# Performance work log

Measured on AMD Instinct MI355X. Metric: run time of the kernel, lower is better.

Reference implementation:

```python
import jax, jax.numpy as jnp
import numpy as np

N_EL = 19        # electrodes per graph (hardcoded in module)
N_EDGES = 342    # 19*18 directed edges per graph, no self-loops
N_GRAPHS = 1800
C_IN = 128
C_OUT = 128


def setup_inputs() -> dict:
    key = jax.random.key(0)
    k1, k2, k3 = jax.random.split(key, 3)
    N = N_GRAPHS * N_EL
    x = jax.random.normal(k1, (N, C_IN), dtype=jnp.float32)
    # block-structured edge_index: same 342-edge pattern in every 19-node graph
    src_b, dst_b = np.nonzero(~np.eye(N_EL, dtype=bool))  # all i != j pairs
    offs = (np.arange(N_GRAPHS) * N_EL)[:, None]
    src = (src_b[None, :] + offs).reshape(-1)
    dst = (dst_b[None, :] + offs).reshape(-1)
    edge_index = jnp.asarray(np.stack([src, dst]), dtype=jnp.int32)  # [2, E]
    # learnable params: edge_weights init 'ones'; GraphConv lin_rel (bias) + lin_root (no bias)
    edge_weights = jnp.ones((N_EDGES,), dtype=jnp.float32)
    W_rel = jax.random.normal(k2, (C_OUT, C_IN), dtype=jnp.float32) * 0.05
    b_rel = jnp.zeros((C_OUT,), dtype=jnp.float32)
    W_root = jax.random.normal(k3, (C_OUT, C_IN), dtype=jnp.float32) * 0.05
    return {"x": x, "edge_index": edge_index, "edge_weights": edge_weights,
            "W_rel": W_rel, "b_rel": b_rel, "W_root": W_root}


def reference(x, edge_index, edge_weights, W_rel, b_rel, W_root):
    # repeat per-graph edge weights across all graphs (torch .repeat == jnp.tile)
    E = edge_index.shape[1]
    rep = jnp.tile(edge_weights, E // edge_weights.shape[0])          # [E]
    src, dst = edge_index[0], edge_index[1]
    # GraphConv message passing: gather source features, scale, scatter-add to targets
    msg = x[src] * rep[:, None]                                       # [E, C_in]
    agg = jax.ops.segment_sum(msg, dst, num_segments=x.shape[0])      # [N, C_in]
    # out = lin_rel(agg) + lin_root(x)
    return agg @ W_rel.T + b_rel + x @ W_root.T
```

## Files before the change

### kernel.cpp

```cpp
#include <hip/hip_runtime.h>
#include <hip/hip_bf16.h>

#define GPB 4
#define ROWS 76
#define MP 80
#define LDK 264
#define EPG 342

typedef short short8 __attribute__((ext_vector_type(8)));
typedef float f32x4  __attribute__((ext_vector_type(4)));

__device__ __forceinline__ unsigned int f2bf(float f) {
    unsigned int u = __float_as_uint(f);
    return (u + 0x7fffu + ((u >> 16) & 1u)) >> 16;
}
__device__ __forceinline__ float bf2f(unsigned int h) {
    return __uint_as_float(h << 16);
}
__device__ __forceinline__ int pk2(float lo, float hi) {
    return (int)(f2bf(lo) | (f2bf(hi) << 16));
}

__global__ __launch_bounds__(256) void graphconv_mfma(
    const float* __restrict__ x,
    const int*   __restrict__ ei,
    const float* __restrict__ ew,
    const float* __restrict__ Wrel,
    const float* __restrict__ brel,
    const float* __restrict__ Wroot,
    float* __restrict__ out,
    int E_total)
{
    __shared__ __align__(16) unsigned short Amat[MP * LDK];
    __shared__ float adj[GPB][19][20];

    const int t    = threadIdx.x;
    const int lane = t & 63;
    const int wv   = t >> 6;
    const int g0   = blockIdx.x * GPB;

    const int lrow = lane & 15;
    const int kq   = (lane >> 4) * 8;
    const int colA = wv * 16 + lrow;
    const int colB = (wv + 4) * 16 + lrow;

    short8 bf[2][2][4];
    #pragma unroll
    for (int pass = 0; pass < 2; ++pass) {
        const float* W = pass ? Wroot : Wrel;
        #pragma unroll
        for (int ct = 0; ct < 2; ++ct) {
            const float* wr = W + (size_t)(ct ? colB : colA) * 128 + kq;
            #pragma unroll
            for (int ks = 0; ks < 4; ++ks) {
                const float4* p = (const float4*)(wr + ks * 32);
                float4 a = p[0], b = p[1];
                union { short8 s; int i[4]; } u;
                u.i[0] = pk2(a.x, a.y); u.i[1] = pk2(a.z, a.w);
                u.i[2] = pk2(b.x, b.y); u.i[3] = pk2(b.z, b.w);
                bf[pass][ct][ks] = u.s;
            }
        }
    }
    const float bias0 = brel[colA];
    const float bias1 = brel[colB];

    const float4* xg = (const float4*)(x + (size_t)g0 * 19 * 128);
    for (int idx = t; idx < ROWS * 32; idx += 256) {
        int row = idx >> 5, c4 = idx & 31;
        float4 v = xg[idx];
        int2 w; w.x = pk2(v.x, v.y); w.y = pk2(v.z, v.w);
        *(int2*)&Amat[row * LDK + 128 + c4 * 4] = w;
    }
    for (int i = t; i < GPB * 19 * 20; i += 256) ((float*)adj)[i] = 0.f;
    __syncthreads();

    for (int e = t; e < GPB * EPG; e += 256) {
        int g  = e / EPG;
        int te = e - g * EPG;
        int ge = g0 * EPG + e;
        int nb = (g0 + g) * 19;
        int sl = ei[ge] - nb;
        int dl = ei[E_total + ge] - nb;
        adj[g][dl][sl] = ew[te];
    }
    __syncthreads();

    for (int idx = t; idx < ROWS * 128; idx += 256) {
        int j = idx >> 7, c = idx & 127;
        int g = j / 19, jl = j - g * 19;
        int bg = g * 19;
        float s = 0.f;
        #pragma unroll
        for (int i = 0; i < 19; ++i)
            s += adj[g][jl][i] * bf2f(Amat[(bg + i) * LDK + 128 + c]);
        Amat[j * LDK + c] = (unsigned short)f2bf(s);
    }
    __syncthreads();

    float* ob = out + (size_t)blockIdx.x * ROWS * 128;
    #pragma unroll
    for (int rt = 0; rt < 5; ++rt) {
        f32x4 acc0 = {0.f, 0.f, 0.f, 0.f};
        f32x4 acc1 = {0.f, 0.f, 0.f, 0.f};
        const unsigned short* ar = Amat + (rt * 16 + lrow) * LDK + kq;
        #pragma unroll
        for (int ks = 0; ks < 8; ++ks) {
            short8 a = *(const short8*)(ar + ks * 32);
            int p = ks >> 2, k4 = ks & 3;
            acc0 = __builtin_amdgcn_mfma_f32_16x16x32_bf16(a, bf[p][0][k4], acc0, 0, 0, 0);
            acc1 = __builtin_amdgcn_mfma_f32_16x16x32_bf16(a, bf[p][1][k4], acc1, 0, 0, 0);
        }
        int rbase = rt * 16 + (lane >> 4) * 4;
        #pragma unroll
        for (int r = 0; r < 4; ++r) {
            int row = rbase + r;
            if (row < ROWS) {
                ob[row * 128 + colA] = acc0[r] + bias0;
                ob[row * 128 + colB] = acc1[r] + bias1;
            }
        }
    }
}

extern "C" void kernel_launch(void* const* d_in, const int* in_sizes, int n_in,
                              void* d_out, int out_size, void* d_ws, size_t ws_size,
                              hipStream_t stream) {
    const float* x     = (const float*)d_in[0];
    const int*   ei    = (const int*)d_in[1];
    const float* ew    = (const float*)d_in[2];
    const float* Wrel  = (const float*)d_in[3];
    const float* brel  = (const float*)d_in[4];
    const float* Wroot = (const float*)d_in[5];
    float* out = (float*)d_out;

    const int E_total  = in_sizes[1] / 2;
    const int n_graphs = E_total / EPG;
    const int n_blocks = n_graphs / GPB;

    graphconv_mfma<<<n_blocks, 256, 0, stream>>>(
        x, ei, ew, Wrel, brel, Wroot, out, E_total);
}
```

Before: 115.3 us.

## Halve graphs per block and vectorize neighbor aggregation over 8 channels

Result: faster. 106.8 us (-7.4%).

```diff
diff --git a/kernel.cpp b/kernel.cpp
--- a/kernel.cpp
+++ b/kernel.cpp
@@ -1,23 +1,20 @@
 #include <hip/hip_runtime.h>
 #include <hip/hip_bf16.h>
 
-#define GPB 4
-#define ROWS 76
-#define MP 80
+#define GPB 2
+#define ROWS 38
+#define MP 48
 #define LDK 264
 #define EPG 342
 
 typedef short short8 __attribute__((ext_vector_type(8)));
 typedef float f32x4  __attribute__((ext_vector_type(4)));
 
-__device__ __forceinline__ unsigned int f2bf(float f) {
+static __device__ __forceinline__ unsigned int f2bf(float f) {
     unsigned int u = __float_as_uint(f);
     return (u + 0x7fffu + ((u >> 16) & 1u)) >> 16;
 }
-__device__ __forceinline__ float bf2f(unsigned int h) {
-    return __uint_as_float(h << 16);
-}
-__device__ __forceinline__ int pk2(float lo, float hi) {
+static __device__ __forceinline__ int pk2(float lo, float hi) {
     return (int)(f2bf(lo) | (f2bf(hi) << 16));
 }
 
@@ -76,7 +73,7 @@
     __syncthreads();
 
     for (int e = t; e < GPB * EPG; e += 256) {
-        int g  = e / EPG;
+        int g  = (e >= EPG) ? 1 : 0;
         int te = e - g * EPG;
         int ge = g0 * EPG + e;
         int nb = (g0 + g) * 19;
@@ -86,21 +83,37 @@
     }
     __syncthreads();
 
-    for (int idx = t; idx < ROWS * 128; idx += 256) {
-        int j = idx >> 7, c = idx & 127;
-        int g = j / 19, jl = j - g * 19;
+    for (int idx = t; idx < ROWS * 16; idx += 256) {
+        int j = idx >> 4, c8 = idx & 15;
+        int g = (j >= 19) ? 1 : 0;
+        int jl = j - g * 19;
         int bg = g * 19;
-        float s = 0.f;
+        float acc[8];
         #pragma unroll
-        for (int i = 0; i < 19; ++i)
-            s += adj[g][jl][i] * bf2f(Amat[(bg + i) * LDK + 128 + c]);
-        Amat[j * LDK + c] = (unsigned short)f2bf(s);
+        for (int q = 0; q < 8; ++q) acc[q] = 0.f;
+        #pragma unroll 4
+        for (int i = 0; i < 19; ++i) {
+            float a = adj[g][jl][i];
+            int4 w = *(const int4*)&Amat[(bg + i) * LDK + 128 + c8 * 8];
+            acc[0] += a * __uint_as_float((unsigned)w.x << 16);
+            acc[1] += a * __uint_as_float((unsigned)w.x & 0xffff0000u);
+            acc[2] += a * __uint_as_float((unsigned)w.y << 16);
+            acc[3] += a * __uint_as_float((unsigned)w.y & 0xffff0000u);
+            acc[4] += a * __uint_as_float((unsigned)w.z << 16);
+            acc[5] += a * __uint_as_float((unsigned)w.z & 0xffff0000u);
+            acc[6] += a * __uint_as_float((unsigned)w.w << 16);
+            acc[7] += a * __uint_as_float((unsigned)w.w & 0xffff0000u);
+        }
+        int4 o;
+        o.x = pk2(acc[0], acc[1]); o.y = pk2(acc[2], acc[3]);
+        o.z = pk2(acc[4], acc[5]); o.w = pk2(acc[6], acc[7]);
+        *(int4*)&Amat[j * LDK + c8 * 8] = o;
     }
     __syncthreads();
 
     float* ob = out + (size_t)blockIdx.x * ROWS * 128;
     #pragma unroll
-    for (int rt = 0; rt < 5; ++rt) {
+    for (int rt = 0; rt < 3; ++rt) {
         f32x4 acc0 = {0.f, 0.f, 0.f, 0.f};
         f32x4 acc1 = {0.f, 0.f, 0.f, 0.f};
         const unsigned short* ar = Amat + (rt * 16 + lrow) * LDK + kq;
```

## Reorder GraphConv as A·(X·Wrel) and precompute bf16 weights in a separate kernel

Applied to the files above, without the earlier changes.

Result: faster. 93.98 us (-18.5%).

```diff
diff --git a/kernel.cpp b/kernel.cpp
--- a/kernel.cpp
+++ b/kernel.cpp
@@ -1,123 +1,161 @@
 #include <hip/hip_runtime.h>
 #include <hip/hip_bf16.h>
 
-#define GPB 4
-#define ROWS 76
-#define MP 80
-#define LDK 264
 #define EPG 342
+#define LDX 136
+#define LDT 72
+#define LDA 40
 
 typedef short short8 __attribute__((ext_vector_type(8)));
 typedef float f32x4  __attribute__((ext_vector_type(4)));
 
-__device__ __forceinline__ unsigned int f2bf(float f) {
+static __device__ __forceinline__ unsigned int f2bf(float f) {
     unsigned int u = __float_as_uint(f);
     return (u + 0x7fffu + ((u >> 16) & 1u)) >> 16;
 }
-__device__ __forceinline__ float bf2f(unsigned int h) {
-    return __uint_as_float(h << 16);
-}
-__device__ __forceinline__ int pk2(float lo, float hi) {
+static __device__ __forceinline__ int pk2(float lo, float hi) {
     return (int)(f2bf(lo) | (f2bf(hi) << 16));
 }
 
-__global__ __launch_bounds__(256) void graphconv_mfma(
+__global__ __launch_bounds__(256) void conv_w(
+    const float* __restrict__ Wrel, const float* __restrict__ Wroot,
+    unsigned short* __restrict__ wsW)
+{
+    int tid = blockIdx.x * 256 + threadIdx.x;
+    const float* src = (tid < 4096) ? (Wrel + tid * 4)
+                                    : (Wroot + (tid - 4096) * 4);
+    float4 v = *(const float4*)src;
+    int2 w; w.x = pk2(v.x, v.y); w.y = pk2(v.z, v.w);
+    *(int2*)&wsW[tid * 4] = w;
+}
+
+__global__ __launch_bounds__(256) void fused(
     const float* __restrict__ x,
     const int*   __restrict__ ei,
     const float* __restrict__ ew,
-    const float* __restrict__ Wrel,
+    const unsigned short* __restrict__ wsW,
     const float* __restrict__ brel,
-    const float* __restrict__ Wroot,
     float* __restrict__ out,
     int E_total)
 {
-    __shared__ __align__(16) unsigned short Amat[MP * LDK];
-    __shared__ float adj[GPB][19][20];
+    __shared__ __align__(16) unsigned short Xs[64 * LDX];
+    __shared__ __align__(16) unsigned short T1T[128 * LDT];
+    __shared__ __align__(16) unsigned short adj[2 * 32 * LDA];
 
     const int t    = threadIdx.x;
     const int lane = t & 63;
     const int wv   = t >> 6;
-    const int g0   = blockIdx.x * GPB;
-
+    const int g0   = blockIdx.x * 2;
     const int lrow = lane & 15;
     const int kq   = (lane >> 4) * 8;
-    const int colA = wv * 16 + lrow;
-    const int colB = (wv + 4) * 16 + lrow;
-
-    short8 bf[2][2][4];
-    #pragma unroll
-    for (int pass = 0; pass < 2; ++pass) {
-        const float* W = pass ? Wroot : Wrel;
-        #pragma unroll
-        for (int ct = 0; ct < 2; ++ct) {
-            const float* wr = W + (size_t)(ct ? colB : colA) * 128 + kq;
-            #pragma unroll
-            for (int ks = 0; ks < 4; ++ks) {
-                const float4* p = (const float4*)(wr + ks * 32);
-                float4 a = p[0], b = p[1];
-                union { short8 s; int i[4]; } u;
-                u.i[0] = pk2(a.x, a.y); u.i[1] = pk2(a.z, a.w);
-                u.i[2] = pk2(b.x, b.y); u.i[3] = pk2(b.z, b.w);
-                bf[pass][ct][ks] = u.s;
-            }
-        }
-    }
-    const float bias0 = brel[colA];
-    const float bias1 = brel[colB];
 
     const float4* xg = (const float4*)(x + (size_t)g0 * 19 * 128);
-    for (int idx = t; idx < ROWS * 32; idx += 256) {
-        int row = idx >> 5, c4 = idx & 31;
-        float4 v = xg[idx];
-        int2 w; w.x = pk2(v.x, v.y); w.y = pk2(v.z, v.w);
-        *(int2*)&Amat[row * LDK + 128 + c4 * 4] = w;
+    float4 xc[5];
+    #pragma unroll
+    for (int q = 0; q < 5; ++q) { int i = t + q * 256; if (i < 1216) xc[q] = xg[i]; }
+
+    short8 wf[4][4];
+    #pragma unroll
+    for (int nl = 0; nl < 4; ++nl) {
+        int col = (wv + nl * 4) * 16 + lrow;
+        #pragma unroll
+        for (int ks = 0; ks < 4; ++ks)
+            wf[nl][ks] = *(const short8*)&wsW[col * 128 + ks * 32 + kq];
     }
-    for (int i = t; i < GPB * 19 * 20; i += 256) ((float*)adj)[i] = 0.f;
-    __syncthreads();
 
-    for (int e = t; e < GPB * EPG; e += 256) {
-        int g  = e / EPG;
-        int te = e - g * EPG;
-        int ge = g0 * EPG + e;
-        int nb = (g0 + g) * 19;
-        int sl = ei[ge] - nb;
-        int dl = ei[E_total + ge] - nb;
-        adj[g][dl][sl] = ew[te];
+    int   e_d[3]; int e_s[3]; float e_w[3];
+    #pragma unroll
+    for (int q = 0; q < 3; ++q) {
+        int e = t + q * 256;
+        if (e < 2 * EPG) {
+            int gg = (e >= EPG);
+            int ge = g0 * EPG + e;
+            e_s[q] = ei[ge] - (g0 + gg) * 19;
+            e_d[q] = ei[E_total + ge] - (g0 + gg) * 19 + gg * 32;
+            e_w[q] = ew[e - gg * EPG];
+        } else e_s[q] = -1;
+    }
+    const float b0 = brel[wv * 16 + lrow];
+    const float b1 = brel[(wv + 4) * 16 + lrow];
+
+    {
+        int4 z = {0, 0, 0, 0};
+        for (int i = t; i < 320; i += 256) ((int4*)adj)[i] = z;
+        for (int i = t; i < 416; i += 256) {
+            int r = i >> 4, c = i & 15;
+            int g = (r >= 13); int lr = 19 + r - g * 13;
+            *(int4*)&Xs[(g * 32 + lr) * LDX + c * 8] = z;
+        }
     }
     __syncthreads();
 
-    for (int idx = t; idx < ROWS * 128; idx += 256) {
-        int j = idx >> 7, c = idx & 127;
-        int g = j / 19, jl = j - g * 19;
-        int bg = g * 19;
-        float s = 0.f;
-        #pragma unroll
-        for (int i = 0; i < 19; ++i)
-            s += adj[g][jl][i] * bf2f(Amat[(bg + i) * LDK + 128 + c]);
-        Amat[j * LDK + c] = (unsigned short)f2bf(s);
+    #pragma unroll
+    for (int q = 0; q < 3; ++q)
+        if (e_s[q] >= 0) adj[e_d[q] * LDA + e_s[q]] = (unsigned short)f2bf(e_w[q]);
+    #pragma unroll
+    for (int q = 0; q < 5; ++q) {
+        int i = t + q * 256;
+        if (i < 1216) {
+            int row = i >> 5, c4 = i & 31;
+            int g = (row >= 19); int lr = row - g * 19;
+            float4 v = xc[q];
+            int2 w; w.x = pk2(v.x, v.y); w.y = pk2(v.z, v.w);
+            *(int2*)&Xs[(g * 32 + lr) * LDX + c4 * 4] = w;
+        }
     }
     __syncthreads();
 
-    float* ob = out + (size_t)blockIdx.x * ROWS * 128;
+    f32x4 acc[4][4];
     #pragma unroll
-    for (int rt = 0; rt < 5; ++rt) {
-        f32x4 acc0 = {0.f, 0.f, 0.f, 0.f};
-        f32x4 acc1 = {0.f, 0.f, 0.f, 0.f};
-        const unsigned short* ar = Amat + (rt * 16 + lrow) * LDK + kq;
+    for (int mt = 0; mt < 4; ++mt)
         #pragma unroll
-        for (int ks = 0; ks < 8; ++ks) {
-            short8 a = *(const short8*)(ar + ks * 32);
-            int p = ks >> 2, k4 = ks & 3;
-            acc0 = __builtin_amdgcn_mfma_f32_16x16x32_bf16(a, bf[p][0][k4], acc0, 0, 0, 0);
-            acc1 = __builtin_amdgcn_mfma_f32_16x16x32_bf16(a, bf[p][1][k4], acc1, 0, 0, 0);
+        for (int nl = 0; nl < 4; ++nl) acc[mt][nl] = (f32x4){0.f, 0.f, 0.f, 0.f};
+
+    #pragma unroll
+    for (int ks = 0; ks < 4; ++ks) {
+        short8 af[4];
+        #pragma unroll
+        for (int mt = 0; mt < 4; ++mt)
+            af[mt] = *(const short8*)&Xs[(mt * 16 + lrow) * LDX + ks * 32 + kq];
+        #pragma unroll
+        for (int mt = 0; mt < 4; ++mt)
+            #pragma unroll
+            for (int nl = 0; nl < 4; ++nl)
+                acc[mt][nl] = __builtin_amdgcn_mfma_f32_16x16x32_bf16(
+                    af[mt], wf[nl][ks], acc[mt][nl], 0, 0, 0);
+    }
+
+    #pragma unroll
+    for (int mt = 0; mt < 4; ++mt)
+        #pragma unroll
+        for (int nl = 0; nl < 2; ++nl) {
+            int col = (wv + nl * 4) * 16 + lrow;
+            int r0  = mt * 16 + (lane >> 4) * 4;
+            f32x4 a = acc[mt][nl];
+            int2 w; w.x = pk2(a[0], a[1]); w.y = pk2(a[2], a[3]);
+            *(int2*)&T1T[col * LDT + r0] = w;
         }
-        int rbase = rt * 16 + (lane >> 4) * 4;
+    __syncthreads();
+
+    #pragma unroll
+    for (int g = 0; g < 2; ++g) {
         #pragma unroll
-        for (int r = 0; r < 4; ++r) {
-            int row = rbase + r;
-            if (row < ROWS) {
-                ob[row * 128 + colA] = acc0[r] + bias0;
-                ob[row * 128 + colB] = acc1[r] + bias1;
+        for (int mt = 0; mt < 2; ++mt) {
+            short8 aa = *(const short8*)&adj[(g * 32 + mt * 16 + lrow) * LDA + kq];
+            #pragma unroll
+            for (int nl = 0; nl < 2; ++nl) {
+                int col = (wv + nl * 4) * 16 + lrow;
+                short8 bb = *(const short8*)&T1T[col * LDT + g * 32 + kq];
+                f32x4 c = acc[g * 2 + mt][nl + 2];
+                c = __builtin_amdgcn_mfma_f32_16x16x32_bf16(aa, bb, c, 0, 0, 0);
+                int m0 = mt * 16 + (lane >> 4) * 4;
+                float bias = nl ? b1 : b0;
+                float* og = out + (size_t)(g0 + g) * 19 * 128 + col;
+                #pragma unroll
+                for (int r = 0; r < 4; ++r) {
+                    int m = m0 + r;
+                    if (m < 19) og[m * 128] = c[r] + bias;
+                }
             }
         }
     }
@@ -133,11 +171,11 @@
     const float* brel  = (const float*)d_in[4];
     const float* Wroot = (const float*)d_in[5];
     float* out = (float*)d_out;
+    unsigned short* wsW = (unsigned short*)d_ws;
 
     const int E_total  = in_sizes[1] / 2;
     const int n_graphs = E_total / EPG;
-    const int n_blocks = n_graphs / GPB;
 
-    graphconv_mfma<<<n_blocks, 256, 0, stream>>>(
-        x, ei, ew, Wrel, brel, Wroot, out, E_total);
+    conv_w<<<32, 256, 0, stream>>>(Wrel, Wroot, wsW);
+    fused<<<n_graphs / 2, 256, 0, stream>>>(x, ei, ew, wsW, brel, out, E_total);
 }
```
